# Kernel optimization log

Measured on AMD Instinct MI355X. Metric: run time of the kernel, lower is better.

## Reference

```python
import jax, jax.numpy as jnp
import numpy as np

B, T, C, H = 8, 4096, 384, 64

def setup_inputs() -> dict:
    key = jax.random.key(0)
    k1, k2, k3, k4 = jax.random.split(key, 4)
    x = jax.random.normal(k1, (B, T, C), dtype=jnp.float32)
    Wq = jax.random.normal(k2, (C, H), dtype=jnp.float32) / np.sqrt(C)
    Wk = jax.random.normal(k3, (C, H), dtype=jnp.float32) / np.sqrt(C)
    Wv = jax.random.normal(k4, (C, H), dtype=jnp.float32) / np.sqrt(C)
    return {"x": x, "Wq": Wq, "Wk": Wk, "Wv": Wv}

def reference(x, Wq, Wk, Wv):
    # single-head causal self-attention (dropout in eval mode = identity)
    T_ = x.shape[1]
    q = jnp.einsum('btc,ch->bth', x, Wq)   # [B,T,H]
    k = jnp.einsum('btc,ch->bth', x, Wk)   # [B,T,H]
    v = jnp.einsum('btc,ch->bth', x, Wv)   # [B,T,H]
    scale = 1.0 / jnp.sqrt(jnp.float32(Wq.shape[1]))
    wei = jnp.einsum('bth,bsh->bts', q, k) * scale        # [B,T,T]
    causal = jnp.tril(jnp.ones((T_, T_), dtype=bool))
    wei = jnp.where(causal, wei, -jnp.inf)
    wei = jax.nn.softmax(wei, axis=-1)
    out = jnp.einsum('bts,bsh->bth', wei, v)              # [B,T,H]
    return out
```

## Files before the change

kernel.cpp:

```cpp
#include <hip/hip_runtime.h>
#include <hip/hip_bf16.h>
#include <cstdint>
#include <cstddef>

#define BATCH 8
#define SEQ   4096
#define CDIM  384
#define HDIM  64

typedef __attribute__((ext_vector_type(8)))  __bf16 bf16x8;
typedef __attribute__((ext_vector_type(4)))  float  f32x4;
typedef __attribute__((ext_vector_type(16))) float  f32x16;
typedef __attribute__((ext_vector_type(4)))  short  short4v;

#if __has_builtin(__builtin_amdgcn_permlane32_swap)
#define HAVE_PERMLANE 1
#else
#define HAVE_PERMLANE 0
#endif

typedef __attribute__((address_space(3))) char lds_char;
typedef const __attribute__((address_space(1))) char gbl_char;

static __device__ __forceinline__ void gl_lds16(const void* g, void* l) {
  __builtin_amdgcn_global_load_lds((gbl_char*)g, (lds_char*)l, 16, 0, 0);
}

static __device__ __forceinline__ short f2bf(float f) {
  union { float f; uint32_t u; } v; v.f = f;
  uint32_t r = v.u + 0x7fffu + ((v.u >> 16) & 1u);
  return (short)(r >> 16);
}

static __device__ __forceinline__ uint32_t cvtpk(float lo, float hi) {
  uint32_t r;
  asm("v_cvt_pk_bf16_f32 %0, %1, %2" : "=v"(r) : "v"(lo), "v"(hi));
  return r;
}

static __device__ __forceinline__ f32x4 mfma16(bf16x8 a, bf16x8 b, f32x4 c) {
  return __builtin_amdgcn_mfma_f32_16x16x32_bf16(a, b, c, 0, 0, 0);
}

static __device__ __forceinline__ f32x16 mfma32(bf16x8 a, bf16x8 b, f32x16 c) {
  return __builtin_amdgcn_mfma_f32_32x32x16_bf16(a, b, c, 0, 0, 0);
}

static __device__ __forceinline__ f32x4 zero4() {
  f32x4 z = {0.f, 0.f, 0.f, 0.f};
  return z;
}

static __device__ __forceinline__ float xhalf(float x, int hi) {
#if HAVE_PERMLANE
  union { float f; uint32_t u; } a; a.f = x;
  auto r = __builtin_amdgcn_permlane32_swap(a.u, a.u, false, false);
  union { uint32_t u; float f; } o; o.u = hi ? r[0] : r[1];
  return o.f;
#else
  return __shfl_xor(x, 32, 64);
#endif
}

static __device__ __forceinline__ void swap32(uint32_t& a, uint32_t& b, int hi) {
#if HAVE_PERMLANE
  auto r = __builtin_amdgcn_permlane32_swap(a, b, false, false);
  a = r[0]; b = r[1];
#else
  uint32_t sa = (uint32_t)__shfl_xor((int)a, 32, 64);
  uint32_t sb = (uint32_t)__shfl_xor((int)b, 32, 64);
  uint32_t na = hi ? sb : a;
  uint32_t nb = hi ? b : sa;
  a = na; b = nb;
#endif
}

__global__ __launch_bounds__(256) void wpack_kernel(
    const float* __restrict__ Wq, const float* __restrict__ Wk,
    const float* __restrict__ Wv, short* __restrict__ Wt) {
  int idx = blockIdx.x * 256 + threadIdx.x;
  if (idx >= 192 * CDIM) return;
  int n = idx / CDIM;
  int c = idx - n * CDIM;
  int m = n >> 6, h = n & 63;
  const float* W = (m == 0) ? Wq : (m == 1) ? Wk : Wv;
  float s = (m == 0) ? 0.18033688011112042f : 1.0f;
  Wt[idx] = f2bf(W[c * HDIM + h] * s);
}

#define XPAD 392

__global__ __launch_bounds__(256) void qkv_kernel(
    const float* __restrict__ x, const short* __restrict__ Wt,
    short* __restrict__ qb, short* __restrict__ kb, short* __restrict__ vT) {
  __shared__ short xs[64 * XPAD];
  const int tid = threadIdx.x;
  const int tokbase = blockIdx.x * 64;

  const float4* xg = (const float4*)(x + (size_t)tokbase * CDIM);
  for (int it = tid; it < 64 * (CDIM / 4); it += 256) {
    int r  = it / (CDIM / 4);
    int c4 = it - r * (CDIM / 4);
    float4 v = xg[it];
    uint2 st;
    st.x = cvtpk(v.x, v.y);
    st.y = cvtpk(v.z, v.w);
    *(uint2*)&xs[r * XPAD + c4 * 4] = st;
  }
  __syncthreads();

  const int wave = tid >> 6;
  const int lane = tid & 63;
  const int l16  = lane & 15;
  const int lq   = lane >> 4;

  f32x4 acc[4][3];
  #pragma unroll
  for (int ai = 0; ai < 4; ++ai)
    #pragma unroll
    for (int j = 0; j < 3; ++j) acc[ai][j] = zero4();

  #pragma unroll 2
  for (int kk = 0; kk < CDIM / 32; ++kk) {
    const int k0 = kk * 32;
    bf16x8 a[4];
    #pragma unroll
    for (int ai = 0; ai < 4; ++ai)
      a[ai] = *(const bf16x8*)&xs[(ai * 16 + l16) * XPAD + k0 + lq * 8];
    bf16x8 bb[3];
    #pragma unroll
    for (int j = 0; j < 3; ++j) {
      const int nt = wave * 3 + j;
      bb[j] = *(const bf16x8*)&Wt[(size_t)(nt * 16 + l16) * CDIM + k0 + lq * 8];
    }
    #pragma unroll
    for (int ai = 0; ai < 4; ++ai)
      #pragma unroll
      for (int j = 0; j < 3; ++j)
        acc[ai][j] = mfma16(a[ai], bb[j], acc[ai][j]);
  }

  const int b     = tokbase >> 12;
  const int tloc0 = tokbase & (SEQ - 1);
  #pragma unroll
  for (int j = 0; j < 3; ++j) {
    const int col = (wave * 3 + j) * 16 + l16;
    const int mat = col >> 6;
    const int h   = col & 63;
    #pragma unroll
    for (int ai = 0; ai < 4; ++ai) {
      const int row0 = ai * 16 + lq * 4;
      if (mat < 2) {
        short* dst = mat ? kb : qb;
        #pragma unroll
        for (int r = 0; r < 4; ++r)
          dst[(size_t)(tokbase + row0 + r) * HDIM + h] = f2bf(acc[ai][j][r]);
      } else {
        union { uint32_t u[2]; short4v s; } sv;
        sv.u[0] = cvtpk(acc[ai][j][0], acc[ai][j][1]);
        sv.u[1] = cvtpk(acc[ai][j][2], acc[ai][j][3]);
        *(short4v*)&vT[(size_t)(b * HDIM + h) * SEQ + (tloc0 + row0)] = sv.s;
      }
    }
  }
}

__global__ __launch_bounds__(256, 3) void attn_kernel(
    const short* __restrict__ qb, const short* __restrict__ kb,
    const short* __restrict__ vT, float* __restrict__ out,
    float* __restrict__ opart, float2* __restrict__ mlw) {
  __shared__ short kvbuf[2][2][4096];

  const int tid  = threadIdx.x;
  const int wave = tid >> 6;
  const int lane = tid & 63;
  const int l31  = lane & 31;
  const int hi   = lane >> 5;
  const int bid  = blockIdx.x;
  const int b    = bid & 7;
  const int idx  = bid >> 3;
  const int qt   = 31 - (idx >> 2);
  const int quarter = idx & 3;
  const int nkv  = 2 * qt + 2;
  const int base = nkv >> 2;
  const int rem  = nkv & 3;
  const int scnt = base + (quarter < rem ? 1 : 0);
  const int sbeg = quarter * base + (quarter < rem ? quarter : rem);
  const int q0   = qt << 7;
  const int qw0  = q0 + wave * 32;
  const size_t bT = (size_t)b * SEQ;

  const char* kg = (const char*)(kb + bT * HDIM);
  const char* vg = (const char*)(vT + (size_t)b * HDIM * SEQ);

  const int rsub = lane >> 3;
  const int gcol = ((lane & 7) << 4) ^ (rsub << 4);
  const int krb  = wave * 16;

  f32x16 oacc[2];
  #pragma unroll
  for (int hb = 0; hb < 2; ++hb)
    #pragma unroll
    for (int r = 0; r < 16; ++r) oacc[hb][r] = 0.f;
  float m = -1e30f, l = 0.f;

  if (scnt > 0) {
    bf16x8 qf[4];
    {
      const short* qrow = qb + (bT + qw0 + l31) * HDIM + hi * 8;
      #pragma unroll
      for (int t = 0; t < 4; ++t)
        qf[t] = *(const bf16x8*)(qrow + 16 * t);
    }
    const int sw = (l31 & 7) << 4;
    int colk[4];
    #pragma unroll
    for (int t = 0; t < 4; ++t) colk[t] = ((t * 32) + hi * 16) ^ sw;
    const int rbase = l31 * 128;

    {
      const int sf = sbeg << 6;
      #pragma unroll
      for (int i = 0; i < 2; ++i) {
        const int r = krb + i * 8;
        gl_lds16(kg + (size_t)(sf + r + rsub) * 128 + gcol,
                 (char*)&kvbuf[0][0][0] + r * 128);
        gl_lds16(vg + (size_t)(r + rsub) * 8192 + (size_t)sf * 2 + gcol,
                 (char*)&kvbuf[0][1][0] + r * 128);
      }
    }
    __syncthreads();

    int cur = 0;
    for (int it = 0; it < scnt; ++it) {
      const int s0 = (sbeg + it) << 6;
      if (it + 1 < scnt) {
        const int s1 = s0 + 64;
        const int nb = cur ^ 1;
        #pragma unroll
        for (int i = 0; i < 2; ++i) {
          const int r = krb + i * 8;
          gl_lds16(kg + (size_t)(s1 + r + rsub) * 128 + gcol,
                   (char*)&kvbuf[nb][0][0] + r * 128);
          gl_lds16(vg + (size_t)(r + rsub) * 8192 + (size_t)s1 * 2 + gcol,
                   (char*)&kvbuf[nb][1][0] + r * 128);
        }
      }

      if (s0 <= qw0 + 31) {
        const char* bufc = (const char*)kvbuf + cur * 16384;

        f32x16 sacc[2];
        #pragma unroll
        for (int sb = 0; sb < 2; ++sb) {
          #pragma unroll
          for (int r = 0; r < 16; ++r) sacc[sb][r] = 0.f;
          #pragma unroll
          for (int t = 0; t < 4; ++t) {
            bf16x8 kf = *(const bf16x8*)(bufc + sb * 4096 + rbase + colk[t]);
            sacc[sb] = mfma32(kf, qf[t], sacc[sb]);
          }
        }

        if (s0 + 63 > qw0) {
          const int qg = qw0 + l31;
          #pragma unroll
          for (int sb = 0; sb < 2; ++sb)
            #pragma unroll
            for (int r = 0; r < 16; ++r) {
              const int sg = s0 + sb * 32 + (r & 3) + 8 * (r >> 2) + 4 * hi;
              if (sg > qg) sacc[sb][r] = -3e38f;
            }
        }

        float pm = sacc[0][0];
        #pragma unroll
        for (int r = 1; r < 16; ++r) pm = fmaxf(pm, sacc[0][r]);
        #pragma unroll
        for (int r = 0; r < 16; ++r) pm = fmaxf(pm, sacc[1][r]);
        pm = fmaxf(pm, xhalf(pm, hi));

        if (!__all(pm <= m + 8.f)) {
          const float mn = fmaxf(m, pm);
          const float sc = exp2f(m - mn);
          m = mn; l *= sc;
          #pragma unroll
          for (int hb = 0; hb < 2; ++hb)
            #pragma unroll
            for (int r = 0; r < 16; ++r) oacc[hb][r] *= sc;
        }

        float p[2][16];
        float rs = 0.f;
        #pragma unroll
        for (int sb = 0; sb < 2; ++sb)
          #pragma unroll
          for (int r = 0; r < 16; ++r) {
            p[sb][r] = exp2f(sacc[sb][r] - m);
            rs += p[sb][r];
          }
        rs += xhalf(rs, hi);
        l += rs;

        uint32_t w[2][4][2];
        #pragma unroll
        for (int sb = 0; sb < 2; ++sb)
          #pragma unroll
          for (int g = 0; g < 4; ++g) {
            w[sb][g][0] = cvtpk(p[sb][4 * g + 0], p[sb][4 * g + 1]);
            w[sb][g][1] = cvtpk(p[sb][4 * g + 2], p[sb][4 * g + 3]);
          }

        bf16x8 pf[4];
        #pragma unroll
        for (int sb = 0; sb < 2; ++sb)
          #pragma unroll
          for (int t = 0; t < 2; ++t) {
            uint32_t a0 = w[sb][2 * t][0], b0 = w[sb][2 * t + 1][0];
            uint32_t a1 = w[sb][2 * t][1], b1 = w[sb][2 * t + 1][1];
            swap32(a0, b0, hi);
            swap32(a1, b1, hi);
            union { uint32_t u[4]; bf16x8 v; } uu;
            uu.u[0] = a0; uu.u[1] = a1; uu.u[2] = b0; uu.u[3] = b1;
            pf[sb * 2 + t] = uu.v;
          }

        __builtin_amdgcn_s_setprio(1);
        #pragma unroll
        for (int hb = 0; hb < 2; ++hb)
          #pragma unroll
          for (int ks = 0; ks < 4; ++ks) {
            bf16x8 vf = *(const bf16x8*)(bufc + 8192 + hb * 4096 + rbase + colk[ks]);
            oacc[hb] = mfma32(vf, pf[ks], oacc[hb]);
          }
        __builtin_amdgcn_s_setprio(0);
      }

      __syncthreads();
      cur ^= 1;
    }
  }

  float* obase = (quarter == 0)
      ? out : opart + (size_t)(quarter - 1) * (BATCH * SEQ * HDIM);
  const int q = qw0 + l31;
  #pragma unroll
  for (int hb = 0; hb < 2; ++hb)
    #pragma unroll
    for (int g = 0; g < 4; ++g) {
      float4 o;
      o.x = oacc[hb][4 * g + 0]; o.y = oacc[hb][4 * g + 1];
      o.z = oacc[hb][4 * g + 2]; o.w = oacc[hb][4 * g + 3];
      const int h0 = hb * 32 + 8 * g + 4 * hi;
      *(float4*)&obase[(bT + q) * HDIM + h0] = o;
    }
  if (lane < 32) {
    float2 ml; ml.x = m; ml.y = l;
    mlw[quarter * (BATCH * SEQ) + bT + q] = ml;
  }
}

__global__ __launch_bounds__(256) void merge_kernel(
    float* __restrict__ out, const float* __restrict__ opart,
    const float2* __restrict__ mlw) {
  const int g   = blockIdx.x * 256 + threadIdx.x;
  const int row = g >> 4;
  const int c4  = (g & 15) << 2;
  const float2 ml0 = mlw[row];
  const float2 ml1 = mlw[BATCH * SEQ + row];
  const float2 ml2 = mlw[2 * BATCH * SEQ + row];
  const float2 ml3 = mlw[3 * BATCH * SEQ + row];
  const float mm = fmaxf(fmaxf(ml0.x, ml1.x), fmaxf(ml2.x, ml3.x));
  const float w0 = exp2f(ml0.x - mm);
  const float w1 = exp2f(ml1.x - mm);
  const float w2 = exp2f(ml2.x - mm);
  const float w3 = exp2f(ml3.x - mm);
  const float inv =
      1.0f / (w0 * ml0.y + w1 * ml1.y + w2 * ml2.y + w3 * ml3.y);
  const size_t off = (size_t)row * HDIM + c4;
  const size_t stride = (size_t)BATCH * SEQ * HDIM;
  float4 a0 = *(const float4*)&out[off];
  float4 a1 = *(const float4*)&opart[off];
  float4 a2 = *(const float4*)&opart[off + stride];
  float4 a3 = *(const float4*)&opart[off + 2 * stride];
  float4 r;
  r.x = (w0 * a0.x + w1 * a1.x + w2 * a2.x + w3 * a3.x) * inv;
  r.y = (w0 * a0.y + w1 * a1.y + w2 * a2.y + w3 * a3.y) * inv;
  r.z = (w0 * a0.z + w1 * a1.z + w2 * a2.z + w3 * a3.z) * inv;
  r.w = (w0 * a0.w + w1 * a1.w + w2 * a2.w + w3 * a3.w) * inv;
  *(float4*)&out[off] = r;
}

extern "C" void kernel_launch(void* const* d_in, const int* in_sizes, int n_in,
                              void* d_out, int out_size, void* d_ws, size_t ws_size,
                              hipStream_t stream) {
  (void)in_sizes; (void)n_in; (void)out_size; (void)ws_size;
  const float* x  = (const float*)d_in[0];
  const float* Wq = (const float*)d_in[1];
  const float* Wk = (const float*)d_in[2];
  const float* Wv = (const float*)d_in[3];

  const size_t qkvb = (size_t)BATCH * SEQ * HDIM * sizeof(short);
  const size_t opb  = (size_t)BATCH * SEQ * HDIM * sizeof(float);
  char* ws = (char*)d_ws;
  short*  qb    = (short*)(ws);
  short*  kb    = (short*)(ws + qkvb);
  short*  vT    = (short*)(ws + 2 * qkvb);
  float*  opart = (float*)(ws + 3 * qkvb);
  float2* mlw   = (float2*)(ws + 3 * qkvb + 3 * opb);
  short*  Wt    = (short*)(ws + 3 * qkvb + 3 * opb +
                           (size_t)4 * BATCH * SEQ * sizeof(float2));

  wpack_kernel<<<dim3((192 * CDIM + 255) / 256), dim3(256), 0, stream>>>(Wq, Wk, Wv, Wt);
  qkv_kernel<<<dim3(BATCH * SEQ / 64), dim3(256), 0, stream>>>(x, Wt, qb, kb, vT);
  attn_kernel<<<dim3(1024), dim3(256), 0, stream>>>(qb, kb, vT, (float*)d_out, opart, mlw);
  merge_kernel<<<dim3(BATCH * SEQ * HDIM / 4 / 256), dim3(256), 0, stream>>>(
      (float*)d_out, opart, mlw);
}
```

Baseline: 74.19 us.

## Split attention KV range eightfold with bf16 partial outputs and chunked QKV staging

Splits each query tile's KV range across eight blocks instead of four, doubling the grid to 2048 blocks for better load balance and occupancy. Partial outputs are now stored in bf16 and all merged in a generalized merge kernel, which cuts partial-output traffic per split but adds precision loss and more merge work. The QKV projection now stages x into LDS in three 128-column chunks with a double buffer, reducing LDS footprint. The max and sum reductions are also rewritten as tree reductions to shorten dependency chains.

```diff
diff --git a/kernel.cpp b/kernel.cpp
--- a/kernel.cpp
+++ b/kernel.cpp
@@ -7,6 +7,7 @@
 #define SEQ   4096
 #define CDIM  384
 #define HDIM  64
+#define NSPL  8
 
 typedef __attribute__((ext_vector_type(8)))  __bf16 bf16x8;
 typedef __attribute__((ext_vector_type(4)))  float  f32x4;
@@ -30,6 +31,12 @@
   union { float f; uint32_t u; } v; v.f = f;
   uint32_t r = v.u + 0x7fffu + ((v.u >> 16) & 1u);
   return (short)(r >> 16);
+}
+
+static __device__ __forceinline__ float bf2f(short s) {
+  union { uint32_t u; float f; } t;
+  t.u = ((uint32_t)(uint16_t)s) << 16;
+  return t.f;
 }
 
 static __device__ __forceinline__ uint32_t cvtpk(float lo, float hi) {
@@ -75,6 +82,14 @@
 #endif
 }
 
+static __device__ __forceinline__ float tmax16(const f32x16& v) {
+  float a = fmaxf(fmaxf(v[0], v[1]), fmaxf(v[2], v[3]));
+  float b = fmaxf(fmaxf(v[4], v[5]), fmaxf(v[6], v[7]));
+  float c = fmaxf(fmaxf(v[8], v[9]), fmaxf(v[10], v[11]));
+  float d = fmaxf(fmaxf(v[12], v[13]), fmaxf(v[14], v[15]));
+  return fmaxf(fmaxf(a, b), fmaxf(c, d));
+}
+
 __global__ __launch_bounds__(256) void wpack_kernel(
     const float* __restrict__ Wq, const float* __restrict__ Wk,
     const float* __restrict__ Wv, short* __restrict__ Wt) {
@@ -88,24 +103,21 @@
   Wt[idx] = f2bf(W[c * HDIM + h] * s);
 }
 
-#define XPAD 392
+#define KPAD 136
 
 __global__ __launch_bounds__(256) void qkv_kernel(
     const float* __restrict__ x, const short* __restrict__ Wt,
     short* __restrict__ qb, short* __restrict__ kb, short* __restrict__ vT) {
-  __shared__ short xs[64 * XPAD];
+  __shared__ short xs[2][64][KPAD];
   const int tid = threadIdx.x;
   const int tokbase = blockIdx.x * 64;
-
   const float4* xg = (const float4*)(x + (size_t)tokbase * CDIM);
-  for (int it = tid; it < 64 * (CDIM / 4); it += 256) {
-    int r  = it / (CDIM / 4);
-    int c4 = it - r * (CDIM / 4);
-    float4 v = xg[it];
-    uint2 st;
-    st.x = cvtpk(v.x, v.y);
-    st.y = cvtpk(v.z, v.w);
-    *(uint2*)&xs[r * XPAD + c4 * 4] = st;
+
+  for (int i = tid; i < 2048; i += 256) {
+    int r = i >> 5, c4 = i & 31;
+    float4 v = xg[r * 96 + c4];
+    uint2 st; st.x = cvtpk(v.x, v.y); st.y = cvtpk(v.z, v.w);
+    *(uint2*)&xs[0][r][c4 * 4] = st;
   }
   __syncthreads();
 
@@ -120,24 +132,38 @@
     #pragma unroll
     for (int j = 0; j < 3; ++j) acc[ai][j] = zero4();
 
-  #pragma unroll 2
-  for (int kk = 0; kk < CDIM / 32; ++kk) {
-    const int k0 = kk * 32;
-    bf16x8 a[4];
-    #pragma unroll
-    for (int ai = 0; ai < 4; ++ai)
-      a[ai] = *(const bf16x8*)&xs[(ai * 16 + l16) * XPAD + k0 + lq * 8];
-    bf16x8 bb[3];
-    #pragma unroll
-    for (int j = 0; j < 3; ++j) {
-      const int nt = wave * 3 + j;
-      bb[j] = *(const bf16x8*)&Wt[(size_t)(nt * 16 + l16) * CDIM + k0 + lq * 8];
-    }
-    #pragma unroll
-    for (int ai = 0; ai < 4; ++ai)
+  for (int ch = 0; ch < 3; ++ch) {
+    if (ch < 2) {
+      const int nb = (ch + 1) & 1;
+      for (int i = tid; i < 2048; i += 256) {
+        int r = i >> 5, c4 = i & 31;
+        float4 v = xg[r * 96 + (ch + 1) * 32 + c4];
+        uint2 st; st.x = cvtpk(v.x, v.y); st.y = cvtpk(v.z, v.w);
+        *(uint2*)&xs[nb][r][c4 * 4] = st;
+      }
+    }
+    const int cb = ch & 1;
+    #pragma unroll
+    for (int kk = 0; kk < 4; ++kk) {
+      const int k0 = kk * 32;
+      bf16x8 a[4];
       #pragma unroll
-      for (int j = 0; j < 3; ++j)
-        acc[ai][j] = mfma16(a[ai], bb[j], acc[ai][j]);
+      for (int ai = 0; ai < 4; ++ai)
+        a[ai] = *(const bf16x8*)&xs[cb][ai * 16 + l16][k0 + lq * 8];
+      bf16x8 bb[3];
+      #pragma unroll
+      for (int j = 0; j < 3; ++j) {
+        const int nt = wave * 3 + j;
+        bb[j] = *(const bf16x8*)&Wt[(size_t)(nt * 16 + l16) * CDIM +
+                                    ch * 128 + k0 + lq * 8];
+      }
+      #pragma unroll
+      for (int ai = 0; ai < 4; ++ai)
+        #pragma unroll
+        for (int j = 0; j < 3; ++j)
+          acc[ai][j] = mfma16(a[ai], bb[j], acc[ai][j]);
+    }
+    __syncthreads();
   }
 
   const int b     = tokbase >> 12;
@@ -167,8 +193,8 @@
 
 __global__ __launch_bounds__(256, 3) void attn_kernel(
     const short* __restrict__ qb, const short* __restrict__ kb,
-    const short* __restrict__ vT, float* __restrict__ out,
-    float* __restrict__ opart, float2* __restrict__ mlw) {
+    const short* __restrict__ vT, short* __restrict__ opart,
+    float2* __restrict__ mlw) {
   __shared__ short kvbuf[2][2][4096];
 
   const int tid  = threadIdx.x;
@@ -179,13 +205,14 @@
   const int bid  = blockIdx.x;
   const int b    = bid & 7;
   const int idx  = bid >> 3;
-  const int qt   = 31 - (idx >> 2);
-  const int quarter = idx & 3;
+  const int qt   = 31 - (idx >> 3);
+  const int part = idx & 7;
   const int nkv  = 2 * qt + 2;
-  const int base = nkv >> 2;
-  const int rem  = nkv & 3;
-  const int scnt = base + (quarter < rem ? 1 : 0);
-  const int sbeg = quarter * base + (quarter < rem ? quarter : rem);
+  const int base = nkv >> 3;
+  const int rem  = nkv & 7;
+  const int scnt = base + (part < rem ? 1 : 0);
+  const int sbeg = part * base + (part < rem ? part : rem);
+  const bool dia = (scnt > 0) && (sbeg + scnt == nkv);
   const int q0   = qt << 7;
   const int qw0  = q0 + wave * 32;
   const size_t bT = (size_t)b * SEQ;
@@ -273,11 +300,7 @@
             }
         }
 
-        float pm = sacc[0][0];
-        #pragma unroll
-        for (int r = 1; r < 16; ++r) pm = fmaxf(pm, sacc[0][r]);
-        #pragma unroll
-        for (int r = 0; r < 16; ++r) pm = fmaxf(pm, sacc[1][r]);
+        float pm = fmaxf(tmax16(sacc[0]), tmax16(sacc[1]));
         pm = fmaxf(pm, xhalf(pm, hi));
 
         if (!__all(pm <= m + 8.f)) {
@@ -291,14 +314,20 @@
         }
 
         float p[2][16];
-        float rs = 0.f;
         #pragma unroll
         for (int sb = 0; sb < 2; ++sb)
           #pragma unroll
-          for (int r = 0; r < 16; ++r) {
+          for (int r = 0; r < 16; ++r)
             p[sb][r] = exp2f(sacc[sb][r] - m);
-            rs += p[sb][r];
-          }
+        float t8[8];
+        #pragma unroll
+        for (int sb = 0; sb < 2; ++sb)
+          #pragma unroll
+          for (int g = 0; g < 4; ++g)
+            t8[sb * 4 + g] = (p[sb][4 * g] + p[sb][4 * g + 1]) +
+                             (p[sb][4 * g + 2] + p[sb][4 * g + 3]);
+        float rs = ((t8[0] + t8[1]) + (t8[2] + t8[3])) +
+                   ((t8[4] + t8[5]) + (t8[6] + t8[7]));
         rs += xhalf(rs, hi);
         l += rs;
 
@@ -341,53 +370,57 @@
     }
   }
 
-  float* obase = (quarter == 0)
-      ? out : opart + (size_t)(quarter - 1) * (BATCH * SEQ * HDIM);
+  short* obase = opart + (size_t)part * ((size_t)BATCH * SEQ * HDIM);
   const int q = qw0 + l31;
   #pragma unroll
   for (int hb = 0; hb < 2; ++hb)
     #pragma unroll
     for (int g = 0; g < 4; ++g) {
-      float4 o;
-      o.x = oacc[hb][4 * g + 0]; o.y = oacc[hb][4 * g + 1];
-      o.z = oacc[hb][4 * g + 2]; o.w = oacc[hb][4 * g + 3];
-      const int h0 = hb * 32 + 8 * g + 4 * hi;
-      *(float4*)&obase[(bT + q) * HDIM + h0] = o;
+      uint2 st;
+      st.x = cvtpk(oacc[hb][4 * g + 0], oacc[hb][4 * g + 1]);
+      st.y = cvtpk(oacc[hb][4 * g + 2], oacc[hb][4 * g + 3]);
+      *(uint2*)&obase[(bT + q) * HDIM + hb * 32 + 8 * g + 4 * hi] = st;
     }
   if (lane < 32) {
     float2 ml; ml.x = m; ml.y = l;
-    mlw[quarter * (BATCH * SEQ) + bT + q] = ml;
+    mlw[part * (BATCH * SEQ) + bT + q] = ml;
   }
 }
 
 __global__ __launch_bounds__(256) void merge_kernel(
-    float* __restrict__ out, const float* __restrict__ opart,
+    float* __restrict__ out, const short* __restrict__ opart,
     const float2* __restrict__ mlw) {
   const int g   = blockIdx.x * 256 + threadIdx.x;
   const int row = g >> 4;
   const int c4  = (g & 15) << 2;
-  const float2 ml0 = mlw[row];
-  const float2 ml1 = mlw[BATCH * SEQ + row];
-  const float2 ml2 = mlw[2 * BATCH * SEQ + row];
-  const float2 ml3 = mlw[3 * BATCH * SEQ + row];
-  const float mm = fmaxf(fmaxf(ml0.x, ml1.x), fmaxf(ml2.x, ml3.x));
-  const float w0 = exp2f(ml0.x - mm);
-  const float w1 = exp2f(ml1.x - mm);
-  const float w2 = exp2f(ml2.x - mm);
-  const float w3 = exp2f(ml3.x - mm);
-  const float inv =
-      1.0f / (w0 * ml0.y + w1 * ml1.y + w2 * ml2.y + w3 * ml3.y);
+  float2 ml[NSPL];
+  float mm = -3.4e38f;
+  #pragma unroll
+  for (int i = 0; i < NSPL; ++i) {
+    ml[i] = mlw[i * (BATCH * SEQ) + row];
+    mm = fmaxf(mm, ml[i].x);
+  }
+  float w[NSPL];
+  float ls = 0.f;
+  #pragma unroll
+  for (int i = 0; i < NSPL; ++i) {
+    w[i] = exp2f(ml[i].x - mm);
+    ls += w[i] * ml[i].y;
+  }
+  const size_t stride = (size_t)BATCH * SEQ * HDIM;
   const size_t off = (size_t)row * HDIM + c4;
-  const size_t stride = (size_t)BATCH * SEQ * HDIM;
-  float4 a0 = *(const float4*)&out[off];
-  float4 a1 = *(const float4*)&opart[off];
-  float4 a2 = *(const float4*)&opart[off + stride];
-  float4 a3 = *(const float4*)&opart[off + 2 * stride];
+  float a0 = 0.f, a1 = 0.f, a2 = 0.f, a3 = 0.f;
+  #pragma unroll
+  for (int i = 0; i < NSPL; ++i) {
+    short4v s = *(const short4v*)&opart[i * stride + off];
+    a0 += w[i] * bf2f(s[0]);
+    a1 += w[i] * bf2f(s[1]);
+    a2 += w[i] * bf2f(s[2]);
+    a3 += w[i] * bf2f(s[3]);
+  }
+  const float inv = 1.0f / ls;
   float4 r;
-  r.x = (w0 * a0.x + w1 * a1.x + w2 * a2.x + w3 * a3.x) * inv;
-  r.y = (w0 * a0.y + w1 * a1.y + w2 * a2.y + w3 * a3.y) * inv;
-  r.z = (w0 * a0.z + w1 * a1.z + w2 * a2.z + w3 * a3.z) * inv;
-  r.w = (w0 * a0.w + w1 * a1.w + w2 * a2.w + w3 * a3.w) * inv;
+  r.x = a0 * inv; r.y = a1 * inv; r.z = a2 * inv; r.w = a3 * inv;
   *(float4*)&out[off] = r;
 }
 
@@ -401,19 +434,19 @@
   const float* Wv = (const float*)d_in[3];
 
   const size_t qkvb = (size_t)BATCH * SEQ * HDIM * sizeof(short);
-  const size_t opb  = (size_t)BATCH * SEQ * HDIM * sizeof(float);
+  const size_t opb  = (size_t)NSPL * BATCH * SEQ * HDIM * sizeof(short);
+  const size_t mlb  = (size_t)NSPL * BATCH * SEQ * sizeof(float2);
   char* ws = (char*)d_ws;
   short*  qb    = (short*)(ws);
   short*  kb    = (short*)(ws + qkvb);
   short*  vT    = (short*)(ws + 2 * qkvb);
-  float*  opart = (float*)(ws + 3 * qkvb);
-  float2* mlw   = (float2*)(ws + 3 * qkvb + 3 * opb);
-  short*  Wt    = (short*)(ws + 3 * qkvb + 3 * opb +
-                           (size_t)4 * BATCH * SEQ * sizeof(float2));
+  short*  opart = (short*)(ws + 3 * qkvb);
+  float2* mlw   = (float2*)(ws + 3 * qkvb + opb);
+  short*  Wt    = (short*)(ws + 3 * qkvb + opb + mlb);
 
   wpack_kernel<<<dim3((192 * CDIM + 255) / 256), dim3(256), 0, stream>>>(Wq, Wk, Wv, Wt);
   qkv_kernel<<<dim3(BATCH * SEQ / 64), dim3(256), 0, stream>>>(x, Wt, qb, kb, vT);
-  attn_kernel<<<dim3(1024), dim3(256), 0, stream>>>(qb, kb, vT, (float*)d_out, opart, mlw);
+  attn_kernel<<<dim3(2048), dim3(256), 0, stream>>>(qb, kb, vT, opart, mlw);
   merge_kernel<<<dim3(BATCH * SEQ * HDIM / 4 / 256), dim3(256), 0, stream>>>(
       (float*)d_out, opart, mlw);
 }
```

Measured after the change: 74.27 us. About the same (+0.1%).
